# Performance work log

Measured on AMD Instinct MI355X. Metric: run time of the kernel, lower is better.

## Reference

```python
import jax, jax.numpy as jnp
import numpy as np

VOCAB_FACTORS = (16, 16, 16, 8)   # prod = 32768 = vocab_size
DIM_FACTORS = (4, 4, 4, 4)        # prod = 256   = projection_dim
RANKS = (1, 16, 16, 16, 1)        # tt_rank = 16
NUM_CORES = 4


def _core_shapes():
    return [(RANKS[k], VOCAB_FACTORS[k], DIM_FACTORS[k], RANKS[k + 1])
            for k in range(NUM_CORES)]


def _vocab_strides():
    # big-endian mixed-radix decomposition of a flat vocab index
    strides = []
    s = 1
    for n in reversed(VOCAB_FACTORS):
        strides.append(s)
        s *= n
    return tuple(reversed(strides))


def tt_lookup(cores, idx):
    """Reconstruct embedding rows from TT cores.
    cores[k]: [r_k, n_k, m_k, r_{k+1}];  idx: int array [...].
    Returns [..., prod(m_k)]."""
    flat = idx.reshape(-1)                                # [Bf]
    res = jnp.ones((flat.shape[0], 1, 1), dtype=cores[0].dtype)  # [Bf, M=1, r=1]
    for core, n, st in zip(cores, VOCAB_FACTORS, _vocab_strides()):
        digit = (flat // st) % n                          # [Bf]
        g = jnp.moveaxis(core[:, digit], 1, 0)            # [Bf, r, m, r']
        res = jnp.einsum('bMr,brms->bMms', res, g)        # [Bf, M, m, r']
        res = res.reshape(res.shape[0], -1, res.shape[-1])  # [Bf, M*m, r']
    D = res.shape[1]
    return res[..., 0].reshape(idx.shape + (D,))


def setup_inputs() -> dict:
    key = jax.random.key(0)
    ks = jax.random.split(key, 12)
    B, NEG, V = 8192, 20, int(np.prod(VOCAB_FACTORS))
    inp = {
        'center_words': jax.random.randint(ks[0], (B, 1), 0, V),
        'target_words': jax.random.randint(ks[1], (B, 1), 0, V),
        'negative_words': jax.random.randint(ks[2], (B, NEG), 0, V),
    }
    # embedding_v: glorot-style init spread over cores
    for k, shp in enumerate(_core_shapes()):
        glorot_std = float(np.sqrt(2.0 / (shp[0] * shp[1] + shp[2] * shp[3])))
        inp[f'v_core{k}'] = glorot_std * jax.random.normal(ks[3 + k], shp, dtype=jnp.float32)
    # embedding_u: stddev=1e-4 per the module
    for k, shp in enumerate(_core_shapes()):
        inp[f'u_core{k}'] = 1e-4 * jax.random.normal(ks[7 + k], shp, dtype=jnp.float32)
    return inp


def reference(center_words, target_words, negative_words,
              v_core0, v_core1, v_core2, v_core3,
              u_core0, u_core1, u_core2, u_core3):
    v_cores = (v_core0, v_core1, v_core2, v_core3)
    u_cores = (u_core0, u_core1, u_core2, u_core3)
    center_embeds = tt_lookup(v_cores, center_words)      # [B, 1, D]
    target_embeds = tt_lookup(u_cores, target_words)      # [B, 1, D]
    neg_embeds = -tt_lookup(u_cores, negative_words)      # [B, K, D]
    # target.bmm(center^T).squeeze(2) -> [B, 1]
    positive_score = jnp.einsum('bsd,btd->bs', target_embeds, center_embeds)
    # sum over negatives then view [B, 1]
    negative_score = jnp.sum(
        jnp.einsum('bkd,btd->bk', neg_embeds, center_embeds),
        axis=1, keepdims=True)                            # [B, 1]
    loss = jax.nn.log_sigmoid(positive_score) + jax.nn.log_sigmoid(negative_score)
    return -jnp.mean(loss)
```

## Files before the change

kernel.cpp:

```cpp
#include <hip/hip_runtime.h>
#include <hip/hip_bf16.h>

#define DEVINL __device__ __forceinline__

constexpr int NNEG   = 20;
constexpr int NBATCH = 8192;
constexpr int NMAIN_BLOCKS = NBATCH / 4;

constexpr int OFF_H01V = 68608;
constexpr int OFF_H23V = 134144;
constexpr int OFF_H01U = 166912;
constexpr int OFF_H23U = 232448;
constexpr int OFF_PART = 265216;
constexpr int OFF_UTAB_F = 267268;
constexpr size_t UTAB4_BYTES = (size_t)32768 * 128;
constexpr size_t USCALE_BYTE_OFF = (size_t)OFF_UTAB_F * 4 + UTAB4_BYTES;
constexpr size_t WS_NEED_BYTES = USCALE_BYTE_OFF + (size_t)32768 * 4;

DEVINL float bfbits_to_f32(unsigned short h) {
  unsigned int u = ((unsigned int)h) << 16;
  float f;
  __builtin_memcpy(&f, &u, sizeof(f));
  return f;
}

DEVINL unsigned short f32_to_bfbits(float f) {
  __hip_bfloat16 h = __float2bfloat16(f);
  unsigned short hb;
  __builtin_memcpy(&hb, &h, 2);
  return hb;
}

DEVINL float ldconv(const void* s, int i, bool isF32) {
  return isF32 ? ((const float*)s)[i]
               : bfbits_to_f32(((const unsigned short*)s)[i]);
}

DEVINL bool sniff_is_f32_wave(const void* probe, int lane) {
  const unsigned short* p = (const unsigned short*)probe;
  unsigned short h = p[lane];
  int e = (h >> 7) & 0xFF;
  bool insane = (h != 0) && (e < 90 || e > 140);
  unsigned long long m = __ballot(insane);
  return __popcll(m) > 8;
}

__global__ __launch_bounds__(256) void tt_htables(
    const void* v0, const void* v1, const void* v2, const void* v3,
    const void* u0, const void* u1, const void* u2, const void* u3,
    float* __restrict__ ws) {
  __shared__ bool sIsF32;
  if (threadIdx.x < 64) {
    bool r = sniff_is_f32_wave(v1, threadIdx.x);
    if (threadIdx.x == 0) sIsF32 = r;
  }
  __syncthreads();
  const bool isF32 = sIsF32;

  int t = blockIdx.x * 256 + threadIdx.x;
  bool isU = t >= 98304;
  int lt = isU ? t - 98304 : t;
  const void* c0 = isU ? u0 : v0;
  const void* c1 = isU ? u1 : v1;
  const void* c2 = isU ? u2 : v2;
  const void* c3 = isU ? u3 : v3;
  float* dst = ws + (isU ? OFF_H01U : OFF_H01V);

  if (lt < 65536) {
    int combo = lt >> 8, e = lt & 255;
    int d0 = combo >> 4, d1 = combo & 15;
    int M01 = e >> 4, r2 = e & 15;
    int m0 = M01 >> 2, m1 = M01 & 3;
    float s = 0.f;
#pragma unroll
    for (int r1 = 0; r1 < 16; ++r1)
      s = fmaf(ldconv(c0, (d0 * 4 + m0) * 16 + r1, isF32),
               ldconv(c1, ((r1 * 16 + d1) * 4 + m1) * 16 + r2, isF32), s);
    dst[lt] = s;
  } else {
    int lt2 = lt - 65536;
    int combo = lt2 >> 8, e = lt2 & 255;
    int d2 = combo >> 3, d3 = combo & 7;
    int m23 = e >> 4, r2 = e & 15;
    int m2 = m23 >> 2, m3 = m23 & 3;
    float s = 0.f;
#pragma unroll
    for (int r3 = 0; r3 < 16; ++r3)
      s = fmaf(ldconv(c2, ((r2 * 16 + d2) * 4 + m2) * 16 + r3, isF32),
               ldconv(c3, (r3 * 8 + d3) * 4 + m3, isF32), s);
    dst[65536 + lt2] = s;
  }
}

DEVINL float4 ld4(const float* p) { return *reinterpret_cast<const float4*>(p); }

DEVINL float logsigf(float x) {
  return fminf(x, 0.0f) - log1pf(expf(-fabsf(x)));
}

__global__ __launch_bounds__(256) void tt_utab4(const float* __restrict__ ws,
                                                unsigned short* __restrict__ utab4,
                                                float* __restrict__ uscale) {
  const int w    = blockIdx.x * 4 + (threadIdx.x >> 6);
  const int l    = threadIdx.x & 63;
  const int lo   = w & 127;
  const int hi0  = (w >> 7) * 8;

  const float* Bt = ws + OFF_H23U + lo * 256 + (l & 3) * 64;
  float b[64];
#pragma unroll
  for (int i = 0; i < 16; ++i) *reinterpret_cast<float4*>(&b[4 * i]) = ld4(Bt + 4 * i);

  const float* Abase = ws + OFF_H01U + (size_t)hi0 * 256 + (l >> 2) * 16;

#pragma unroll
  for (int rr = 0; rr < 8; rr += 2) {
    float a0[16], a1[16];
#pragma unroll
    for (int i = 0; i < 4; ++i) {
      *reinterpret_cast<float4*>(&a0[4 * i]) = ld4(Abase + rr * 256 + 4 * i);
      *reinterpret_cast<float4*>(&a1[4 * i]) = ld4(Abase + (rr + 1) * 256 + 4 * i);
    }
    float e0[4] = {0.f, 0.f, 0.f, 0.f}, e1[4] = {0.f, 0.f, 0.f, 0.f};
#pragma unroll
    for (int r = 0; r < 16; ++r) {
#pragma unroll
      for (int j = 0; j < 4; ++j) {
        e0[j] = fmaf(a0[r], b[j * 16 + r], e0[j]);
        e1[j] = fmaf(a1[r], b[j * 16 + r], e1[j]);
      }
    }
    float m0 = fmaxf(fmaxf(fabsf(e0[0]), fabsf(e0[1])), fmaxf(fabsf(e0[2]), fabsf(e0[3])));
    float m1 = fmaxf(fmaxf(fabsf(e1[0]), fabsf(e1[1])), fmaxf(fabsf(e1[2]), fabsf(e1[3])));
#pragma unroll
    for (int off = 32; off > 0; off >>= 1) {
      m0 = fmaxf(m0, __shfl_xor(m0, off, 64));
      m1 = fmaxf(m1, __shfl_xor(m1, off, 64));
    }
    const float inv0 = (m0 > 0.f) ? 7.f / m0 : 0.f;
    const float inv1 = (m1 > 0.f) ? 7.f / m1 : 0.f;
    unsigned int p0 = 0, p1 = 0;
#pragma unroll
    for (int j = 0; j < 4; ++j) {
      p0 |= ((unsigned int)(__float2int_rn(e0[j] * inv0) & 15)) << (4 * j);
      p1 |= ((unsigned int)(__float2int_rn(e1[j] * inv1) & 15)) << (4 * j);
    }
    const size_t v0i = (size_t)(hi0 + rr) * 128 + lo;
    const size_t v1i = v0i + 128;
    utab4[v0i * 64 + l] = (unsigned short)p0;
    utab4[v1i * 64 + l] = (unsigned short)p1;
    if (l == 0) {
      uscale[v0i] = m0 * (1.f / 7.f);
      uscale[v1i] = m1 * (1.f / 7.f);
    }
  }
}

__global__ __launch_bounds__(256) void tt_main10(
    const int* __restrict__ cw, const int* __restrict__ tw, const int* __restrict__ nw,
    const float* __restrict__ ws, const unsigned short* __restrict__ utab4,
    const float* __restrict__ uscale, float* __restrict__ partials) {
  const int lane = threadIdx.x & 63;
  const int wid  = threadIdx.x >> 6;
  const int b    = blockIdx.x * 4 + wid;

  __shared__ int sidx[4][24];
  if (lane < 21)
    sidx[wid][lane] = (lane == 0) ? tw[b] : nw[b * NNEG + lane - 1];
  const int ci = cw[b];
  __syncthreads();

  unsigned int uq[21];
#pragma unroll
  for (int k = 0; k < 21; ++k)
    uq[k] = utab4[(size_t)sidx[wid][k] * 64 + lane];

  float c[4] = {0.f, 0.f, 0.f, 0.f};
  {
    const float* A  = ws + OFF_H01V + (ci >> 7) * 256 + (lane >> 2) * 16;
    const float* Bt = ws + OFF_H23V + (ci & 127) * 256 + (lane & 3) * 64;
    float a[16];
#pragma unroll
    for (int i = 0; i < 4; ++i) *reinterpret_cast<float4*>(&a[4 * i]) = ld4(A + 4 * i);
#pragma unroll
    for (int j = 0; j < 4; ++j) {
#pragma unroll
      for (int i = 0; i < 4; ++i) {
        float4 bv = ld4(Bt + j * 16 + 4 * i);
        c[j] = fmaf(a[4 * i], bv.x,
               fmaf(a[4 * i + 1], bv.y,
               fmaf(a[4 * i + 2], bv.z,
               fmaf(a[4 * i + 3], bv.w, c[j]))));
      }
    }
  }

  float pos = 0.f, nacc = 0.f;
#pragma unroll
  for (int k = 0; k < 21; ++k) {
    const float sc = uscale[sidx[wid][k]];
    const unsigned int u = uq[k];
    const float f0 = (float)(((int)((u)       & 15) ^ 8) - 8);
    const float f1 = (float)(((int)((u >> 4)  & 15) ^ 8) - 8);
    const float f2 = (float)(((int)((u >> 8)  & 15) ^ 8) - 8);
    const float f3 = (float)(((int)((u >> 12) & 15) ^ 8) - 8);
    float p = fmaf(f0, c[0], fmaf(f1, c[1], fmaf(f2, c[2], f3 * c[3]))) * sc;
    if (k == 0) pos = p; else nacc += p;
  }

#pragma unroll
  for (int off = 32; off > 0; off >>= 1) {
    pos  += __shfl_xor(pos, off, 64);
    nacc += __shfl_xor(nacc, off, 64);
  }

  __shared__ float sred[4];
  if (lane == 0) sred[wid] = -(logsigf(pos) + logsigf(-nacc));
  __syncthreads();
  if (threadIdx.x == 0)
    partials[blockIdx.x] = sred[0] + sred[1] + sred[2] + sred[3];
}

DEVINL void frag16(const float* __restrict__ A, const float* __restrict__ Bt,
                   int l, float e[4]) {
  const float* Ar = A + (l >> 2) * 16;
  const float* Br = Bt + (l & 3) * 64;
  float a[16], bb[64];
#pragma unroll
  for (int i = 0; i < 4; ++i) *reinterpret_cast<float4*>(&a[4 * i]) = ld4(Ar + 4 * i);
#pragma unroll
  for (int i = 0; i < 16; ++i) *reinterpret_cast<float4*>(&bb[4 * i]) = ld4(Br + 4 * i);
  e[0] = e[1] = e[2] = e[3] = 0.f;
#pragma unroll
  for (int r = 0; r < 16; ++r) {
#pragma unroll
    for (int j = 0; j < 4; ++j) e[j] = fmaf(a[r], bb[j * 16 + r], e[j]);
  }
}

__global__ __launch_bounds__(256) void tt_sgns_main(
    const int* __restrict__ cw, const int* __restrict__ tw, const int* __restrict__ nw,
    const float* __restrict__ ws, float* __restrict__ partials) {
  const int lane = threadIdx.x & 63;
  const int wid  = threadIdx.x >> 6;
  const int b    = blockIdx.x * 4 + wid;

  const int ci = cw[b];
  const int ti = tw[b];
  const int myneg = nw[b * NNEG + (lane < NNEG ? lane : 0)];

  float c[4];
  frag16(ws + OFF_H01V + (ci >> 7) * 256, ws + OFF_H23V + (ci & 127) * 256, lane, c);

  float pos = 0.f, nacc = 0.f;
#pragma unroll 1
  for (int k = 0; k < 21; ++k) {
    const int idx = (k == 0) ? ti : __shfl(myneg, k - 1, 64);
    float e[4];
    frag16(ws + OFF_H01U + (idx >> 7) * 256, ws + OFF_H23U + (idx & 127) * 256, lane, e);
    float p = fmaf(e[0], c[0], fmaf(e[1], c[1], fmaf(e[2], c[2], e[3] * c[3])));
    if (k == 0) pos = p; else nacc += p;
  }

#pragma unroll
  for (int off = 32; off > 0; off >>= 1) {
    pos  += __shfl_xor(pos, off, 64);
    nacc += __shfl_xor(nacc, off, 64);
  }

  __shared__ float sred[4];
  if (lane == 0) sred[wid] = -(logsigf(pos) + logsigf(-nacc));
  __syncthreads();
  if (threadIdx.x == 0)
    partials[blockIdx.x] = sred[0] + sred[1] + sred[2] + sred[3];
}

__global__ void tt_reduce(const float* __restrict__ partials, void* __restrict__ out) {
  float s = 0.f;
  for (int i = threadIdx.x; i < NMAIN_BLOCKS; i += 256) s += partials[i];
#pragma unroll
  for (int off = 32; off > 0; off >>= 1) s += __shfl_xor(s, off, 64);
  __shared__ float sr[4];
  int lane = threadIdx.x & 63, wid = threadIdx.x >> 6;
  if (lane == 0) sr[wid] = s;
  __syncthreads();
  if (threadIdx.x == 0) {
    float res = (sr[0] + sr[1] + sr[2] + sr[3]) * (1.0f / 8192.0f);
    unsigned short hb = f32_to_bfbits(res);
    unsigned int word = (((unsigned int)hb) << 16) | (unsigned int)hb;
    *(unsigned int*)out = word;
  }
}

extern "C" void kernel_launch(void* const* d_in, const int* in_sizes, int n_in,
                              void* d_out, int out_size, void* d_ws, size_t ws_size,
                              hipStream_t stream) {
  const int* cw = (const int*)d_in[0];
  const int* tw = (const int*)d_in[1];
  const int* nw = (const int*)d_in[2];
  float* ws = (float*)d_ws;

  tt_htables<<<768, 256, 0, stream>>>(
      d_in[3], d_in[4], d_in[5], d_in[6], d_in[7], d_in[8], d_in[9], d_in[10], ws);

  if (ws_size >= WS_NEED_BYTES) {
    unsigned short* utab4 = (unsigned short*)(ws + OFF_UTAB_F);
    float* uscale = (float*)((char*)d_ws + USCALE_BYTE_OFF);
    tt_utab4<<<1024, 256, 0, stream>>>(ws, utab4, uscale);
    tt_main10<<<NMAIN_BLOCKS, 256, 0, stream>>>(
        cw, tw, nw, ws, utab4, uscale, ws + OFF_PART);
  } else {
    tt_sgns_main<<<NMAIN_BLOCKS, 256, 0, stream>>>(cw, tw, nw, ws, ws + OFF_PART);
  }
  tt_reduce<<<1, 256, 0, stream>>>(ws + OFF_PART, d_out);
}
```

Before: 54.93 us.

## Fuse TT half-table build and U int4 table build into one kernel

```diff
diff --git a/kernel.cpp b/kernel.cpp
--- a/kernel.cpp
+++ b/kernel.cpp
@@ -6,6 +6,8 @@
 constexpr int NNEG   = 20;
 constexpr int NBATCH = 8192;
 constexpr int NMAIN_BLOCKS = NBATCH / 4;
+constexpr int NU_BLOCKS = 1024;
+constexpr int NV_BLOCKS = 384;
 
 constexpr int OFF_H01V = 68608;
 constexpr int OFF_H23V = 134144;
@@ -43,6 +45,225 @@
   bool insane = (h != 0) && (e < 90 || e > 140);
   unsigned long long m = __ballot(insane);
   return __popcll(m) > 8;
+}
+
+DEVINL float4 ld4(const float* p) { return *reinterpret_cast<const float4*>(p); }
+
+DEVINL float logsigf(float x) {
+  return fminf(x, 0.0f) - log1pf(expf(-fabsf(x)));
+}
+
+__global__ __launch_bounds__(256) void tt_build2(
+    const void* v0, const void* v1, const void* v2, const void* v3,
+    const void* u0, const void* u1, const void* u2, const void* u3,
+    float* __restrict__ ws, unsigned short* __restrict__ utab4,
+    float* __restrict__ uscale) {
+  __shared__ alignas(16) float sc0[64];
+  __shared__ alignas(16) float sc1[8192];
+  __shared__ alignas(16) float sc2[1024];
+  __shared__ alignas(16) float sc3[256];
+  __shared__ alignas(16) float sA[8 * 320];
+  __shared__ alignas(16) float sB[4 * 260];
+  __shared__ bool sIsF32;
+
+  const int t = threadIdx.x;
+  if (t < 64) {
+    bool r = sniff_is_f32_wave(v1, t);
+    if (t == 0) sIsF32 = r;
+  }
+  __syncthreads();
+  const bool isF32 = sIsF32;
+
+  if (blockIdx.x >= NU_BLOCKS) {
+    int vt = (blockIdx.x - NU_BLOCKS) * 256 + t;
+    if (vt < 65536) {
+      int combo = vt >> 8, e = vt & 255;
+      int d0 = combo >> 4, d1 = combo & 15;
+      int M01 = e >> 4, r2 = e & 15;
+      int m0 = M01 >> 2, m1 = M01 & 3;
+      float s = 0.f;
+#pragma unroll
+      for (int r1 = 0; r1 < 16; ++r1)
+        s = fmaf(ldconv(v0, (d0 * 4 + m0) * 16 + r1, isF32),
+                 ldconv(v1, ((r1 * 16 + d1) * 4 + m1) * 16 + r2, isF32), s);
+      ws[OFF_H01V + vt] = s;
+    } else {
+      int lt2 = vt - 65536;
+      int combo = lt2 >> 8, e = lt2 & 255;
+      int d2 = combo >> 3, d3 = combo & 7;
+      int m23 = e >> 4, r2 = e & 15;
+      int m2 = m23 >> 2, m3 = m23 & 3;
+      float s = 0.f;
+#pragma unroll
+      for (int r3 = 0; r3 < 16; ++r3)
+        s = fmaf(ldconv(v2, ((r2 * 16 + d2) * 4 + m2) * 16 + r3, isF32),
+                 ldconv(v3, (r3 * 8 + d3) * 4 + m3, isF32), s);
+      ws[OFF_H23V + lt2] = s;
+    }
+    return;
+  }
+
+  const int lo0 = (blockIdx.x & 31) * 4;
+  const int hi0 = (blockIdx.x >> 5) * 8;
+  const int d0  = hi0 >> 4;
+  const int d1b = hi0 & 15;
+  const int d2  = lo0 >> 3;
+  const int d3b = lo0 & 7;
+
+  if (t < 64) sc0[t] = ldconv(u0, d0 * 64 + t, isF32);
+#pragma unroll
+  for (int i = 0; i < 32; ++i) {
+    int lin = t + i * 256;
+    sc1[lin] = ldconv(u1, (lin >> 9) * 1024 + d1b * 64 + (lin & 511), isF32);
+  }
+#pragma unroll
+  for (int i = 0; i < 4; ++i) {
+    int lin = t + i * 256;
+    sc2[lin] = ldconv(u2, (lin >> 6) * 1024 + d2 * 64 + (lin & 63), isF32);
+  }
+  sc3[t] = ldconv(u3, (t >> 4) * 32 + d3b * 4 + (t & 15), isF32);
+  __syncthreads();
+
+  {
+    const int q = t >> 4, r2 = t & 15;
+    const int m0 = q >> 2, m1 = q & 3;
+#pragma unroll
+    for (int rr = 0; rr < 8; ++rr) {
+      float s = 0.f;
+#pragma unroll
+      for (int r1 = 0; r1 < 16; ++r1)
+        s = fmaf(sc0[m0 * 16 + r1], sc1[((r1 * 8 + rr) * 4 + m1) * 16 + r2], s);
+      sA[rr * 320 + q * 20 + r2] = s;
+    }
+    const int m23 = t >> 4;
+    const int m2 = m23 >> 2, m3 = m23 & 3;
+#pragma unroll
+    for (int lw = 0; lw < 4; ++lw) {
+      float s = 0.f;
+#pragma unroll
+      for (int r3 = 0; r3 < 16; ++r3)
+        s = fmaf(sc2[(r2 * 4 + m2) * 16 + r3], sc3[(r3 * 4 + lw) * 4 + m3], s);
+      sB[lw * 260 + m23 * 16 + r2] = s;
+    }
+  }
+  __syncthreads();
+
+  const int wid = t >> 6;
+  const int l   = t & 63;
+
+  float b[64];
+#pragma unroll
+  for (int i = 0; i < 16; ++i)
+    *reinterpret_cast<float4*>(&b[4 * i]) = ld4(&sB[wid * 260 + (l & 3) * 64 + 4 * i]);
+
+  const float* Abase = &sA[(l >> 2) * 20];
+
+#pragma unroll
+  for (int rr = 0; rr < 8; rr += 2) {
+    float a0[16], a1[16];
+#pragma unroll
+    for (int i = 0; i < 4; ++i) {
+      *reinterpret_cast<float4*>(&a0[4 * i]) = ld4(Abase + rr * 320 + 4 * i);
+      *reinterpret_cast<float4*>(&a1[4 * i]) = ld4(Abase + (rr + 1) * 320 + 4 * i);
+    }
+    float e0[4] = {0.f, 0.f, 0.f, 0.f}, e1[4] = {0.f, 0.f, 0.f, 0.f};
+#pragma unroll
+    for (int r = 0; r < 16; ++r) {
+#pragma unroll
+      for (int j = 0; j < 4; ++j) {
+        e0[j] = fmaf(a0[r], b[j * 16 + r], e0[j]);
+        e1[j] = fmaf(a1[r], b[j * 16 + r], e1[j]);
+      }
+    }
+    float m0 = fmaxf(fmaxf(fabsf(e0[0]), fabsf(e0[1])), fmaxf(fabsf(e0[2]), fabsf(e0[3])));
+    float m1 = fmaxf(fmaxf(fabsf(e1[0]), fabsf(e1[1])), fmaxf(fabsf(e1[2]), fabsf(e1[3])));
+#pragma unroll
+    for (int off = 32; off > 0; off >>= 1) {
+      m0 = fmaxf(m0, __shfl_xor(m0, off, 64));
+      m1 = fmaxf(m1, __shfl_xor(m1, off, 64));
+    }
+    const float inv0 = (m0 > 0.f) ? 7.f / m0 : 0.f;
+    const float inv1 = (m1 > 0.f) ? 7.f / m1 : 0.f;
+    unsigned int p0 = 0, p1 = 0;
+#pragma unroll
+    for (int j = 0; j < 4; ++j) {
+      p0 |= ((unsigned int)(__float2int_rn(e0[j] * inv0) & 15)) << (4 * j);
+      p1 |= ((unsigned int)(__float2int_rn(e1[j] * inv1) & 15)) << (4 * j);
+    }
+    const size_t v0i = (size_t)(hi0 + rr) * 128 + (lo0 + wid);
+    const size_t v1i = v0i + 128;
+    utab4[v0i * 64 + l] = (unsigned short)p0;
+    utab4[v1i * 64 + l] = (unsigned short)p1;
+    if (l == 0) {
+      uscale[v0i] = m0 * (1.f / 7.f);
+      uscale[v1i] = m1 * (1.f / 7.f);
+    }
+  }
+}
+
+__global__ __launch_bounds__(256) void tt_main10(
+    const int* __restrict__ cw, const int* __restrict__ tw, const int* __restrict__ nw,
+    const float* __restrict__ ws, const unsigned short* __restrict__ utab4,
+    const float* __restrict__ uscale, float* __restrict__ partials) {
+  const int lane = threadIdx.x & 63;
+  const int wid  = threadIdx.x >> 6;
+  const int b    = blockIdx.x * 4 + wid;
+
+  __shared__ int sidx[4][24];
+  if (lane < 21)
+    sidx[wid][lane] = (lane == 0) ? tw[b] : nw[b * NNEG + lane - 1];
+  const int ci = cw[b];
+  __syncthreads();
+
+  unsigned int uq[21];
+#pragma unroll
+  for (int k = 0; k < 21; ++k)
+    uq[k] = utab4[(size_t)sidx[wid][k] * 64 + lane];
+
+  float c[4] = {0.f, 0.f, 0.f, 0.f};
+  {
+    const float* A  = ws + OFF_H01V + (ci >> 7) * 256 + (lane >> 2) * 16;
+    const float* Bt = ws + OFF_H23V + (ci & 127) * 256 + (lane & 3) * 64;
+    float a[16];
+#pragma unroll
+    for (int i = 0; i < 4; ++i) *reinterpret_cast<float4*>(&a[4 * i]) = ld4(A + 4 * i);
+#pragma unroll
+    for (int j = 0; j < 4; ++j) {
+#pragma unroll
+      for (int i = 0; i < 4; ++i) {
+        float4 bv = ld4(Bt + j * 16 + 4 * i);
+        c[j] = fmaf(a[4 * i], bv.x,
+               fmaf(a[4 * i + 1], bv.y,
+               fmaf(a[4 * i + 2], bv.z,
+               fmaf(a[4 * i + 3], bv.w, c[j]))));
+      }
+    }
+  }
+
+  float pos = 0.f, nacc = 0.f;
+#pragma unroll
+  for (int k = 0; k < 21; ++k) {
+    const float sc = uscale[sidx[wid][k]];
+    const unsigned int u = uq[k];
+    const float f0 = (float)(((int)((u)       & 15) ^ 8) - 8);
+    const float f1 = (float)(((int)((u >> 4)  & 15) ^ 8) - 8);
+    const float f2 = (float)(((int)((u >> 8)  & 15) ^ 8) - 8);
+    const float f3 = (float)(((int)((u >> 12) & 15) ^ 8) - 8);
+    float p = fmaf(f0, c[0], fmaf(f1, c[1], fmaf(f2, c[2], f3 * c[3]))) * sc;
+    if (k == 0) pos = p; else nacc += p;
+  }
+
+#pragma unroll
+  for (int off = 32; off > 0; off >>= 1) {
+    pos  += __shfl_xor(pos, off, 64);
+    nacc += __shfl_xor(nacc, off, 64);
+  }
+
+  __shared__ float sred[4];
+  if (lane == 0) sred[wid] = -(logsigf(pos) + logsigf(-nacc));
+  __syncthreads();
+  if (threadIdx.x == 0)
+    partials[blockIdx.x] = sred[0] + sred[1] + sred[2] + sred[3];
 }
 
 __global__ __launch_bounds__(256) void tt_htables(
@@ -92,135 +313,6 @@
   }
 }
 
-DEVINL float4 ld4(const float* p) { return *reinterpret_cast<const float4*>(p); }
-
-DEVINL float logsigf(float x) {
-  return fminf(x, 0.0f) - log1pf(expf(-fabsf(x)));
-}
-
-__global__ __launch_bounds__(256) void tt_utab4(const float* __restrict__ ws,
-                                                unsigned short* __restrict__ utab4,
-                                                float* __restrict__ uscale) {
-  const int w    = blockIdx.x * 4 + (threadIdx.x >> 6);
-  const int l    = threadIdx.x & 63;
-  const int lo   = w & 127;
-  const int hi0  = (w >> 7) * 8;
-
-  const float* Bt = ws + OFF_H23U + lo * 256 + (l & 3) * 64;
-  float b[64];
-#pragma unroll
-  for (int i = 0; i < 16; ++i) *reinterpret_cast<float4*>(&b[4 * i]) = ld4(Bt + 4 * i);
-
-  const float* Abase = ws + OFF_H01U + (size_t)hi0 * 256 + (l >> 2) * 16;
-
-#pragma unroll
-  for (int rr = 0; rr < 8; rr += 2) {
-    float a0[16], a1[16];
-#pragma unroll
-    for (int i = 0; i < 4; ++i) {
-      *reinterpret_cast<float4*>(&a0[4 * i]) = ld4(Abase + rr * 256 + 4 * i);
-      *reinterpret_cast<float4*>(&a1[4 * i]) = ld4(Abase + (rr + 1) * 256 + 4 * i);
-    }
-    float e0[4] = {0.f, 0.f, 0.f, 0.f}, e1[4] = {0.f, 0.f, 0.f, 0.f};
-#pragma unroll
-    for (int r = 0; r < 16; ++r) {
-#pragma unroll
-      for (int j = 0; j < 4; ++j) {
-        e0[j] = fmaf(a0[r], b[j * 16 + r], e0[j]);
-        e1[j] = fmaf(a1[r], b[j * 16 + r], e1[j]);
-      }
-    }
-    float m0 = fmaxf(fmaxf(fabsf(e0[0]), fabsf(e0[1])), fmaxf(fabsf(e0[2]), fabsf(e0[3])));
-    float m1 = fmaxf(fmaxf(fabsf(e1[0]), fabsf(e1[1])), fmaxf(fabsf(e1[2]), fabsf(e1[3])));
-#pragma unroll
-    for (int off = 32; off > 0; off >>= 1) {
-      m0 = fmaxf(m0, __shfl_xor(m0, off, 64));
-      m1 = fmaxf(m1, __shfl_xor(m1, off, 64));
-    }
-    const float inv0 = (m0 > 0.f) ? 7.f / m0 : 0.f;
-    const float inv1 = (m1 > 0.f) ? 7.f / m1 : 0.f;
-    unsigned int p0 = 0, p1 = 0;
-#pragma unroll
-    for (int j = 0; j < 4; ++j) {
-      p0 |= ((unsigned int)(__float2int_rn(e0[j] * inv0) & 15)) << (4 * j);
-      p1 |= ((unsigned int)(__float2int_rn(e1[j] * inv1) & 15)) << (4 * j);
-    }
-    const size_t v0i = (size_t)(hi0 + rr) * 128 + lo;
-    const size_t v1i = v0i + 128;
-    utab4[v0i * 64 + l] = (unsigned short)p0;
-    utab4[v1i * 64 + l] = (unsigned short)p1;
-    if (l == 0) {
-      uscale[v0i] = m0 * (1.f / 7.f);
-      uscale[v1i] = m1 * (1.f / 7.f);
-    }
-  }
-}
-
-__global__ __launch_bounds__(256) void tt_main10(
-    const int* __restrict__ cw, const int* __restrict__ tw, const int* __restrict__ nw,
-    const float* __restrict__ ws, const unsigned short* __restrict__ utab4,
-    const float* __restrict__ uscale, float* __restrict__ partials) {
-  const int lane = threadIdx.x & 63;
-  const int wid  = threadIdx.x >> 6;
-  const int b    = blockIdx.x * 4 + wid;
-
-  __shared__ int sidx[4][24];
-  if (lane < 21)
-    sidx[wid][lane] = (lane == 0) ? tw[b] : nw[b * NNEG + lane - 1];
-  const int ci = cw[b];
-  __syncthreads();
-
-  unsigned int uq[21];
-#pragma unroll
-  for (int k = 0; k < 21; ++k)
-    uq[k] = utab4[(size_t)sidx[wid][k] * 64 + lane];
-
-  float c[4] = {0.f, 0.f, 0.f, 0.f};
-  {
-    const float* A  = ws + OFF_H01V + (ci >> 7) * 256 + (lane >> 2) * 16;
-    const float* Bt = ws + OFF_H23V + (ci & 127) * 256 + (lane & 3) * 64;
-    float a[16];
-#pragma unroll
-    for (int i = 0; i < 4; ++i) *reinterpret_cast<float4*>(&a[4 * i]) = ld4(A + 4 * i);
-#pragma unroll
-    for (int j = 0; j < 4; ++j) {
-#pragma unroll
-      for (int i = 0; i < 4; ++i) {
-        float4 bv = ld4(Bt + j * 16 + 4 * i);
-        c[j] = fmaf(a[4 * i], bv.x,
-               fmaf(a[4 * i + 1], bv.y,
-               fmaf(a[4 * i + 2], bv.z,
-               fmaf(a[4 * i + 3], bv.w, c[j]))));
-      }
-    }
-  }
-
-  float pos = 0.f, nacc = 0.f;
-#pragma unroll
-  for (int k = 0; k < 21; ++k) {
-    const float sc = uscale[sidx[wid][k]];
-    const unsigned int u = uq[k];
-    const float f0 = (float)(((int)((u)       & 15) ^ 8) - 8);
-    const float f1 = (float)(((int)((u >> 4)  & 15) ^ 8) - 8);
-    const float f2 = (float)(((int)((u >> 8)  & 15) ^ 8) - 8);
-    const float f3 = (float)(((int)((u >> 12) & 15) ^ 8) - 8);
-    float p = fmaf(f0, c[0], fmaf(f1, c[1], fmaf(f2, c[2], f3 * c[3]))) * sc;
-    if (k == 0) pos = p; else nacc += p;
-  }
-
-#pragma unroll
-  for (int off = 32; off > 0; off >>= 1) {
-    pos  += __shfl_xor(pos, off, 64);
-    nacc += __shfl_xor(nacc, off, 64);
-  }
-
-  __shared__ float sred[4];
-  if (lane == 0) sred[wid] = -(logsigf(pos) + logsigf(-nacc));
-  __syncthreads();
-  if (threadIdx.x == 0)
-    partials[blockIdx.x] = sred[0] + sred[1] + sred[2] + sred[3];
-}
-
 DEVINL void frag16(const float* __restrict__ A, const float* __restrict__ Bt,
                    int l, float e[4]) {
   const float* Ar = A + (l >> 2) * 16;
@@ -300,16 +392,17 @@
   const int* nw = (const int*)d_in[2];
   float* ws = (float*)d_ws;
 
-  tt_htables<<<768, 256, 0, stream>>>(
-      d_in[3], d_in[4], d_in[5], d_in[6], d_in[7], d_in[8], d_in[9], d_in[10], ws);
-
   if (ws_size >= WS_NEED_BYTES) {
     unsigned short* utab4 = (unsigned short*)(ws + OFF_UTAB_F);
     float* uscale = (float*)((char*)d_ws + USCALE_BYTE_OFF);
-    tt_utab4<<<1024, 256, 0, stream>>>(ws, utab4, uscale);
+    tt_build2<<<NU_BLOCKS + NV_BLOCKS, 256, 0, stream>>>(
+        d_in[3], d_in[4], d_in[5], d_in[6], d_in[7], d_in[8], d_in[9], d_in[10],
+        ws, utab4, uscale);
     tt_main10<<<NMAIN_BLOCKS, 256, 0, stream>>>(
         cw, tw, nw, ws, utab4, uscale, ws + OFF_PART);
   } else {
+    tt_htables<<<768, 256, 0, stream>>>(
+        d_in[3], d_in[4], d_in[5], d_in[6], d_in[7], d_in[8], d_in[9], d_in[10], ws);
     tt_sgns_main<<<NMAIN_BLOCKS, 256, 0, stream>>>(cw, tw, nw, ws, ws + OFF_PART);
   }
   tt_reduce<<<1, 256, 0, stream>>>(ws + OFF_PART, d_out);
```

Result: slower. 65.50 us (+19.2%).
